# Kernel optimization log

Measured on AMD Instinct MI355X. Metric: run time of the kernel, lower is better.

Reference implementation:

```python
import jax, jax.numpy as jnp
import numpy as np

NUM_HEADS = 64  # from init_kwargs


def _rx(theta):
    # RX(theta) = [[cos(t/2), -i sin(t/2)], [-i sin(t/2), cos(t/2)]]
    theta = jnp.asarray(theta, jnp.float32)
    c = jnp.cos(theta / 2)
    s = jnp.sin(theta / 2)
    return jnp.stack([jnp.stack([c + 0j, -1j * s], -1),
                      jnp.stack([-1j * s, c + 0j], -1)], -2).astype(jnp.complex64)


def _ry(theta):
    # RY(theta) = [[cos(t/2), -sin(t/2)], [sin(t/2), cos(t/2)]]
    theta = jnp.asarray(theta, jnp.float32)
    c = jnp.cos(theta / 2)
    s = jnp.sin(theta / 2)
    return jnp.stack([jnp.stack([c + 0j, -s + 0j], -1),
                      jnp.stack([s + 0j, c + 0j], -1)], -2).astype(jnp.complex64)


def _apply_1q(state, U, wire):
    # state: (N, 2, 2, ..., 2) with wire w on axis 1+w (torchquantum convention)
    s = jnp.moveaxis(state, 1 + wire, -1)
    if U.ndim == 2:
        s = jnp.einsum('...i,ji->...j', s, U)
    else:  # per-sample gate, U: (N, 2, 2)
        s = jnp.einsum('n...i,nji->n...j', s, U)
    return jnp.moveaxis(s, -1, 1 + wire)


def _cnot(state, c, t):
    s = jnp.moveaxis(state, (1 + c, 1 + t), (-2, -1))
    s = s.at[..., 1, :].set(s[..., 1, ::-1])  # flip target where control==1
    return jnp.moveaxis(s, (-2, -1), (1 + c, 1 + t))


def _qlayer(xf, qparams):
    # xf: (N, d_k) angles; simulates RX-encode, per-wire RY/RX, CNOT ring, PauliZ expvals
    N, dk = xf.shape
    state = jnp.zeros((N, 2 ** dk), jnp.complex64).at[:, 0].set(1.0)
    state = state.reshape((N,) + (2,) * dk)
    for i in range(dk):                      # GeneralEncoder: RX(x_i) on wire i
        state = _apply_1q(state, _rx(xf[:, i]), i)
    for i in range(dk):                      # variational RY, RX per wire
        state = _apply_1q(state, _ry(qparams[i, 0]), i)
        state = _apply_1q(state, _rx(qparams[i, 1]), i)
    for i in range(dk - 1):                  # CNOT chain
        state = _cnot(state, i, i + 1)
    state = _cnot(state, dk - 1, 0)          # ring closure
    probs = state.real ** 2 + state.imag ** 2  # (N, 2,..,2)
    probs = probs.reshape(N, -1)
    # wire w is bit (dk-1-w) of the flattened index (wire 0 = MSB)
    bits = ((jnp.arange(2 ** dk)[:, None] >> jnp.arange(dk - 1, -1, -1)[None, :]) & 1).astype(jnp.float32)
    return probs @ (1.0 - 2.0 * bits)        # (N, dk) PauliZ expectations


def setup_inputs() -> dict:
    key = jax.random.key(0)
    ks = jax.random.split(key, 6)
    B, T, E, dk = 2, 512, 384, 384 // NUM_HEADS
    sc = 1.0 / np.sqrt(E)
    return {
        'x': jax.random.normal(ks[0], (B, T, E), jnp.float32),
        'Wq': jax.random.normal(ks[1], (E, E), jnp.float32) * sc,
        'bq': jnp.zeros((E,), jnp.float32),
        'Wk': jax.random.normal(ks[2], (E, E), jnp.float32) * sc,
        'bk': jnp.zeros((E,), jnp.float32),
        'Wv': jax.random.normal(ks[3], (E, E), jnp.float32) * sc,
        'bv': jnp.zeros((E,), jnp.float32),
        'Wo': jax.random.normal(ks[4], (E, E), jnp.float32) * sc,
        'bo': jnp.zeros((E,), jnp.float32),
        'qparams': jax.random.normal(ks[5], (dk, 2), jnp.float32),
    }


def reference(x, Wq, bq, Wk, bk, Wv, bv, Wo, bo, qparams):
    B, T, E = x.shape
    H = NUM_HEADS
    dk = E // H

    def heads(y):  # (B,T,E) -> (B,H,T,dk)
        return y.reshape(B, T, H, dk).transpose(0, 2, 1, 3)

    q = heads(x @ Wq.T + bq)
    k = heads(x @ Wk.T + bk)
    v = heads(x @ Wv.T + bv)

    def apply_q(layer):
        flat = layer.reshape(-1, dk)
        return _qlayer(flat, qparams).reshape(B, H, T, dk)

    qq, kq, vq = apply_q(q), apply_q(k), apply_q(v)
    scores = jnp.einsum('bhtd,bhsd->bhts', qq, kq) / jnp.sqrt(jnp.float32(dk))
    attn = jax.nn.softmax(scores, axis=-1)
    out = jnp.einsum('bhts,bhsd->bhtd', attn, vq)
    merged = out.transpose(0, 2, 1, 3).reshape(B, T, E)
    return merged @ Wo.T + bo
```

## Files before the change

### kernel.cpp

```cpp
#include <hip/hip_runtime.h>
#include <math.h>

#define SEQ_T   512
#define E_DIM   384
#define H_NUM   64
#define DKQ     6
#define NROWS   1024
#define QKV_ELEMS (NROWS*E_DIM)

__device__ __forceinline__ void qmap6(const float* __restrict__ in,
                                      const float* __restrict__ AB,
                                      float* __restrict__ out)
{
    float z[6];
#pragma unroll
    for (int i = 0; i < 6; ++i) {
        float s, c;
        sincosf(in[i], &s, &c);
        z[i] = AB[i] * c - AB[6 + i] * s;
    }
    float z01 = z[0] * z[1];
    float z12 = z[1] * z[2];
    float z34 = z[3] * z[4];
    out[0] = z12 * z34 * z[5];
    out[1] = z01;
    out[2] = z01 * z[2];
    out[3] = out[2] * z[3];
    out[4] = out[3] * z[4];
    out[5] = out[4] * z[5];
}

__global__ __launch_bounds__(256)
void qkv_gemm(const float* __restrict__ x,
              const float* __restrict__ Wq, const float* __restrict__ bq,
              const float* __restrict__ Wk, const float* __restrict__ bk,
              const float* __restrict__ Wv, const float* __restrict__ bv,
              float* __restrict__ qb, float* __restrict__ kb, float* __restrict__ vb)
{
    __shared__ float xs[64][65];
    __shared__ float ws[64][65];
    const int tid = threadIdx.x;
    const int tx = tid & 15;
    const int ty = tid >> 4;
    const int n0 = blockIdx.x * 64;
    const int j0 = blockIdx.y * 64;

    const float* W; const float* bias; float* ob; int e0;
    if (j0 < 384)      { W = Wq; bias = bq; ob = qb; e0 = j0; }
    else if (j0 < 768) { W = Wk; bias = bk; ob = kb; e0 = j0 - 384; }
    else               { W = Wv; bias = bv; ob = vb; e0 = j0 - 768; }

    float acc[4][4];
#pragma unroll
    for (int i = 0; i < 4; ++i)
#pragma unroll
        for (int j = 0; j < 4; ++j) acc[i][j] = 0.f;

    const int lrow = tid >> 4;
    const int lk   = (tid & 15) << 2;

    for (int kc = 0; kc < E_DIM; kc += 64) {
#pragma unroll
        for (int rr = 0; rr < 4; ++rr) {
            const int row = lrow + rr * 16;
            float4 xv = *reinterpret_cast<const float4*>(x + (size_t)(n0 + row) * E_DIM + kc + lk);
            xs[row][lk + 0] = xv.x; xs[row][lk + 1] = xv.y;
            xs[row][lk + 2] = xv.z; xs[row][lk + 3] = xv.w;
            float4 wv = *reinterpret_cast<const float4*>(W + (size_t)(e0 + row) * E_DIM + kc + lk);
            ws[row][lk + 0] = wv.x; ws[row][lk + 1] = wv.y;
            ws[row][lk + 2] = wv.z; ws[row][lk + 3] = wv.w;
        }
        __syncthreads();
#pragma unroll 8
        for (int kk = 0; kk < 64; ++kk) {
            float a0 = xs[ty * 4 + 0][kk], a1 = xs[ty * 4 + 1][kk];
            float a2 = xs[ty * 4 + 2][kk], a3 = xs[ty * 4 + 3][kk];
            float b0 = ws[tx * 4 + 0][kk], b1 = ws[tx * 4 + 1][kk];
            float b2 = ws[tx * 4 + 2][kk], b3 = ws[tx * 4 + 3][kk];
            acc[0][0] += a0 * b0; acc[0][1] += a0 * b1; acc[0][2] += a0 * b2; acc[0][3] += a0 * b3;
            acc[1][0] += a1 * b0; acc[1][1] += a1 * b1; acc[1][2] += a1 * b2; acc[1][3] += a1 * b3;
            acc[2][0] += a2 * b0; acc[2][1] += a2 * b1; acc[2][2] += a2 * b2; acc[2][3] += a2 * b3;
            acc[3][0] += a3 * b0; acc[3][1] += a3 * b1; acc[3][2] += a3 * b2; acc[3][3] += a3 * b3;
        }
        __syncthreads();
    }

#pragma unroll
    for (int i = 0; i < 4; ++i) {
        const int n = n0 + ty * 4 + i;
        const int b = n >> 9;
        const int t = n & 511;
#pragma unroll
        for (int j = 0; j < 4; ++j) {
            const int e = e0 + tx * 4 + j;
            const int h = e / 6;
            const int d = e - h * 6;
            const float v = acc[i][j] + bias[e];
            ob[(((size_t)(b * H_NUM + h) * SEQ_T) + t) * DKQ + d] = v;
        }
    }
}

__global__ __launch_bounds__(256)
void attn_kernel(const float* __restrict__ qb,
                 const float* __restrict__ kb,
                 const float* __restrict__ vb,
                 const float* __restrict__ qparams,
                 float* __restrict__ merged)
{
    __shared__ __align__(16) float kv[SEQ_T][12];

    const int bh  = blockIdx.x;
    const int tid = threadIdx.x;

    float AB[12];
#pragma unroll
    for (int i = 0; i < 6; ++i) {
        const float a = qparams[i * 2 + 0];
        const float b = qparams[i * 2 + 1];
        AB[i]     = cosf(a) * cosf(b);
        AB[6 + i] = sinf(b);
    }

    const float* Kp = kb + (size_t)bh * SEQ_T * DKQ;
    const float* Vp = vb + (size_t)bh * SEQ_T * DKQ;

    const int t = blockIdx.y * 256 + tid;
    float qin[6];
    const float* Qp = qb + ((size_t)bh * SEQ_T + t) * DKQ;
#pragma unroll
    for (int i = 0; i < 6; ++i) qin[i] = Qp[i];

    {
        const int p = tid;
        const float4* K4 = reinterpret_cast<const float4*>(Kp);
        const float4* V4 = reinterpret_cast<const float4*>(Vp);
        float4 ka = K4[3 * p + 0], kbv = K4[3 * p + 1], kc = K4[3 * p + 2];
        float4 va = V4[3 * p + 0], vbv = V4[3 * p + 1], vc = V4[3 * p + 2];

        float in0[6] = {ka.x, ka.y, ka.z, ka.w, kbv.x, kbv.y};
        float in1[6] = {kbv.z, kbv.w, kc.x, kc.y, kc.z, kc.w};
        float iv0[6] = {va.x, va.y, va.z, va.w, vbv.x, vbv.y};
        float iv1[6] = {vbv.z, vbv.w, vc.x, vc.y, vc.z, vc.w};
        float ok0[6], ok1[6], ov0[6], ov1[6];
        qmap6(in0, AB, ok0); qmap6(in1, AB, ok1);
        qmap6(iv0, AB, ov0); qmap6(iv1, AB, ov1);

        float4* kv4 = reinterpret_cast<float4*>(&kv[0][0]);
        kv4[3 * (2 * p) + 0] = make_float4(ok0[0], ok0[1], ok0[2], ok0[3]);
        kv4[3 * (2 * p) + 1] = make_float4(ok0[4], ok0[5], ov0[0], ov0[1]);
        kv4[3 * (2 * p) + 2] = make_float4(ov0[2], ov0[3], ov0[4], ov0[5]);
        kv4[3 * (2 * p + 1) + 0] = make_float4(ok1[0], ok1[1], ok1[2], ok1[3]);
        kv4[3 * (2 * p + 1) + 1] = make_float4(ok1[4], ok1[5], ov1[0], ov1[1]);
        kv4[3 * (2 * p + 1) + 2] = make_float4(ov1[2], ov1[3], ov1[4], ov1[5]);
    }
    __syncthreads();

    float qrow[6];
    qmap6(qin, AB, qrow);
    const float inv_sqrt_dk = 0.40824829046386296f;
#pragma unroll
    for (int i = 0; i < 6; ++i) qrow[i] *= inv_sqrt_dk;

    float accv[6] = {0.f, 0.f, 0.f, 0.f, 0.f, 0.f};
    float denom = 0.f;

    const float4* kv4 = reinterpret_cast<const float4*>(&kv[0][0]);
#pragma unroll 4
    for (int s = 0; s < SEQ_T; ++s) {
        const float4 r0 = kv4[3 * s + 0];
        const float4 r1 = kv4[3 * s + 1];
        const float4 r2 = kv4[3 * s + 2];
        const float sc = qrow[0] * r0.x + qrow[1] * r0.y + qrow[2] * r0.z
                       + qrow[3] * r0.w + qrow[4] * r1.x + qrow[5] * r1.y;
        const float e = __expf(sc);
        denom += e;
        accv[0] += e * r1.z; accv[1] += e * r1.w;
        accv[2] += e * r2.x; accv[3] += e * r2.y;
        accv[4] += e * r2.z; accv[5] += e * r2.w;
    }

    const float r = 1.0f / denom;
    const int b = bh >> 6;
    const int h = bh & 63;
    float* mp = merged + ((size_t)(b * SEQ_T + t)) * E_DIM + h * DKQ;
#pragma unroll
    for (int d = 0; d < 6; ++d) mp[d] = accv[d] * r;
}

__global__ __launch_bounds__(256)
void out_gemm(const float* __restrict__ merged,
              const float* __restrict__ Wo, const float* __restrict__ bo,
              float* __restrict__ out)
{
    __shared__ float xs[64][65];
    __shared__ float ws[64][65];
    const int tid = threadIdx.x;
    const int tx = tid & 15;
    const int ty = tid >> 4;
    const int n0 = blockIdx.x * 64;
    const int e0 = blockIdx.y * 64;

    float acc[4][4];
#pragma unroll
    for (int i = 0; i < 4; ++i)
#pragma unroll
        for (int j = 0; j < 4; ++j) acc[i][j] = 0.f;

    const int lrow = tid >> 4;
    const int lk   = (tid & 15) << 2;

    for (int kc = 0; kc < E_DIM; kc += 64) {
#pragma unroll
        for (int rr = 0; rr < 4; ++rr) {
            const int row = lrow + rr * 16;
            float4 xv = *reinterpret_cast<const float4*>(merged + (size_t)(n0 + row) * E_DIM + kc + lk);
            xs[row][lk + 0] = xv.x; xs[row][lk + 1] = xv.y;
            xs[row][lk + 2] = xv.z; xs[row][lk + 3] = xv.w;
            float4 wv = *reinterpret_cast<const float4*>(Wo + (size_t)(e0 + row) * E_DIM + kc + lk);
            ws[row][lk + 0] = wv.x; ws[row][lk + 1] = wv.y;
            ws[row][lk + 2] = wv.z; ws[row][lk + 3] = wv.w;
        }
        __syncthreads();
#pragma unroll 8
        for (int kk = 0; kk < 64; ++kk) {
            float a0 = xs[ty * 4 + 0][kk], a1 = xs[ty * 4 + 1][kk];
            float a2 = xs[ty * 4 + 2][kk], a3 = xs[ty * 4 + 3][kk];
            float b0 = ws[tx * 4 + 0][kk], b1 = ws[tx * 4 + 1][kk];
            float b2 = ws[tx * 4 + 2][kk], b3 = ws[tx * 4 + 3][kk];
            acc[0][0] += a0 * b0; acc[0][1] += a0 * b1; acc[0][2] += a0 * b2; acc[0][3] += a0 * b3;
            acc[1][0] += a1 * b0; acc[1][1] += a1 * b1; acc[1][2] += a1 * b2; acc[1][3] += a1 * b3;
            acc[2][0] += a2 * b0; acc[2][1] += a2 * b1; acc[2][2] += a2 * b2; acc[2][3] += a2 * b3;
            acc[3][0] += a3 * b0; acc[3][1] += a3 * b1; acc[3][2] += a3 * b2; acc[3][3] += a3 * b3;
        }
        __syncthreads();
    }

#pragma unroll
    for (int i = 0; i < 4; ++i) {
        const int n = n0 + ty * 4 + i;
#pragma unroll
        for (int j = 0; j < 4; ++j) {
            const int e = e0 + tx * 4 + j;
            out[(size_t)n * E_DIM + e] = acc[i][j] + bo[e];
        }
    }
}

extern "C" void kernel_launch(void* const* d_in, const int* in_sizes, int n_in,
                              void* d_out, int out_size, void* d_ws, size_t ws_size,
                              hipStream_t stream)
{
    const float* x  = (const float*)d_in[0];
    const float* Wq = (const float*)d_in[1];
    const float* bq = (const float*)d_in[2];
    const float* Wk = (const float*)d_in[3];
    const float* bk = (const float*)d_in[4];
    const float* Wv = (const float*)d_in[5];
    const float* bv = (const float*)d_in[6];
    const float* Wo = (const float*)d_in[7];
    const float* bo = (const float*)d_in[8];
    const float* qp = (const float*)d_in[9];
    float* out = (float*)d_out;

    float* qb     = (float*)d_ws;
    float* kb     = qb + QKV_ELEMS;
    float* vb     = kb + QKV_ELEMS;
    float* merged = vb + QKV_ELEMS;

    qkv_gemm<<<dim3(16, 18), 256, 0, stream>>>(x, Wq, bq, Wk, bk, Wv, bv, qb, kb, vb);
    attn_kernel<<<dim3(128, 2), 256, 0, stream>>>(qb, kb, vb, qp, merged);
    out_gemm<<<dim3(16, 6), 256, 0, stream>>>(merged, Wo, bo, out);
}
```

Measured before the change: 165.3 us.

## Split attention over key chunks, precompute quantum map, retile GEMMs to 32x48

Both GEMMs are retiled to 32x48 outputs per 64-thread block with transposed shared-memory layouts and vector loads, which raises the block count and aligns output columns to whole heads for vectorized stores. The quantum map is applied once in a separate in-place pass over qb, kb and vb, so attention no longer recomputes it per block. Attention becomes a split-K design: each block handles a 128-key chunk for all 512 queries and writes partial sums, and a reduce kernel combines the chunks without max subtraction. This adds two kernel launches and a round trip of partial sums through global memory in exchange for more parallelism.

```diff
diff --git a/kernel.cpp b/kernel.cpp
--- a/kernel.cpp
+++ b/kernel.cpp
@@ -7,6 +7,7 @@
 #define DKQ     6
 #define NROWS   1024
 #define QKV_ELEMS (NROWS*E_DIM)
+#define NCHUNK  4
 
 __device__ __forceinline__ void qmap6(const float* __restrict__ in,
                                       const float* __restrict__ AB,
@@ -30,89 +31,114 @@
     out[5] = out[4] * z[5];
 }
 
-__global__ __launch_bounds__(256)
+__device__ __forceinline__ void gemm_32x48(const float* __restrict__ A,
+                                           const float* __restrict__ W,
+                                           int n0, int e0,
+                                           float (&xs)[64][36], float (&ws)[64][52],
+                                           float (&acc)[4][6])
+{
+    const int tid = threadIdx.x;
+    const int tx = tid & 7;
+    const int ty = tid >> 3;
+
+#pragma unroll
+    for (int i = 0; i < 4; ++i)
+#pragma unroll
+        for (int j = 0; j < 6; ++j) acc[i][j] = 0.f;
+
+    for (int kc = 0; kc < E_DIM; kc += 64) {
+#pragma unroll
+        for (int w = 0; w < 8; ++w) {
+            const int idx = tid + 64 * w;
+            const int row = idx & 31;
+            const int kf  = idx >> 5;
+            const float4 g = *reinterpret_cast<const float4*>(
+                A + (size_t)(n0 + row) * E_DIM + kc + kf * 4);
+            xs[kf * 4 + 0][row] = g.x;
+            xs[kf * 4 + 1][row] = g.y;
+            xs[kf * 4 + 2][row] = g.z;
+            xs[kf * 4 + 3][row] = g.w;
+        }
+#pragma unroll
+        for (int w = 0; w < 12; ++w) {
+            const int idx = tid + 64 * w;
+            const int c  = idx % 48;
+            const int kf = idx / 48;
+            const float4 g = *reinterpret_cast<const float4*>(
+                W + (size_t)(e0 + c) * E_DIM + kc + kf * 4);
+            ws[kf * 4 + 0][c] = g.x;
+            ws[kf * 4 + 1][c] = g.y;
+            ws[kf * 4 + 2][c] = g.z;
+            ws[kf * 4 + 3][c] = g.w;
+        }
+        __syncthreads();
+
+#pragma unroll 8
+        for (int kk = 0; kk < 64; ++kk) {
+            const float4 a = *reinterpret_cast<const float4*>(&xs[kk][ty * 4]);
+            const float2 b0 = *reinterpret_cast<const float2*>(&ws[kk][tx * 6 + 0]);
+            const float2 b1 = *reinterpret_cast<const float2*>(&ws[kk][tx * 6 + 2]);
+            const float2 b2 = *reinterpret_cast<const float2*>(&ws[kk][tx * 6 + 4]);
+            const float av[4] = {a.x, a.y, a.z, a.w};
+            const float bv[6] = {b0.x, b0.y, b1.x, b1.y, b2.x, b2.y};
+#pragma unroll
+            for (int i = 0; i < 4; ++i)
+#pragma unroll
+                for (int j = 0; j < 6; ++j) acc[i][j] += av[i] * bv[j];
+        }
+        __syncthreads();
+    }
+}
+
+__global__ __launch_bounds__(64)
 void qkv_gemm(const float* __restrict__ x,
               const float* __restrict__ Wq, const float* __restrict__ bq,
               const float* __restrict__ Wk, const float* __restrict__ bk,
               const float* __restrict__ Wv, const float* __restrict__ bv,
               float* __restrict__ qb, float* __restrict__ kb, float* __restrict__ vb)
 {
-    __shared__ float xs[64][65];
-    __shared__ float ws[64][65];
-    const int tid = threadIdx.x;
-    const int tx = tid & 15;
-    const int ty = tid >> 4;
-    const int n0 = blockIdx.x * 64;
-    const int j0 = blockIdx.y * 64;
-
-    const float* W; const float* bias; float* ob; int e0;
-    if (j0 < 384)      { W = Wq; bias = bq; ob = qb; e0 = j0; }
-    else if (j0 < 768) { W = Wk; bias = bk; ob = kb; e0 = j0 - 384; }
-    else               { W = Wv; bias = bv; ob = vb; e0 = j0 - 768; }
-
-    float acc[4][4];
-#pragma unroll
-    for (int i = 0; i < 4; ++i)
-#pragma unroll
-        for (int j = 0; j < 4; ++j) acc[i][j] = 0.f;
-
-    const int lrow = tid >> 4;
-    const int lk   = (tid & 15) << 2;
-
-    for (int kc = 0; kc < E_DIM; kc += 64) {
-#pragma unroll
-        for (int rr = 0; rr < 4; ++rr) {
-            const int row = lrow + rr * 16;
-            float4 xv = *reinterpret_cast<const float4*>(x + (size_t)(n0 + row) * E_DIM + kc + lk);
-            xs[row][lk + 0] = xv.x; xs[row][lk + 1] = xv.y;
-            xs[row][lk + 2] = xv.z; xs[row][lk + 3] = xv.w;
-            float4 wv = *reinterpret_cast<const float4*>(W + (size_t)(e0 + row) * E_DIM + kc + lk);
-            ws[row][lk + 0] = wv.x; ws[row][lk + 1] = wv.y;
-            ws[row][lk + 2] = wv.z; ws[row][lk + 3] = wv.w;
-        }
-        __syncthreads();
-#pragma unroll 8
-        for (int kk = 0; kk < 64; ++kk) {
-            float a0 = xs[ty * 4 + 0][kk], a1 = xs[ty * 4 + 1][kk];
-            float a2 = xs[ty * 4 + 2][kk], a3 = xs[ty * 4 + 3][kk];
-            float b0 = ws[tx * 4 + 0][kk], b1 = ws[tx * 4 + 1][kk];
-            float b2 = ws[tx * 4 + 2][kk], b3 = ws[tx * 4 + 3][kk];
-            acc[0][0] += a0 * b0; acc[0][1] += a0 * b1; acc[0][2] += a0 * b2; acc[0][3] += a0 * b3;
-            acc[1][0] += a1 * b0; acc[1][1] += a1 * b1; acc[1][2] += a1 * b2; acc[1][3] += a1 * b3;
-            acc[2][0] += a2 * b0; acc[2][1] += a2 * b1; acc[2][2] += a2 * b2; acc[2][3] += a2 * b3;
-            acc[3][0] += a3 * b0; acc[3][1] += a3 * b1; acc[3][2] += a3 * b2; acc[3][3] += a3 * b3;
-        }
-        __syncthreads();
-    }
+    __shared__ __align__(16) float xs[64][36];
+    __shared__ __align__(16) float ws[64][52];
+
+    const int n0 = blockIdx.x * 32;
+    const int by = blockIdx.y;
+    const int sel = by >> 3;
+    const int e0 = (by & 7) * 48;
+
+    const float* W; const float* bias; float* ob;
+    if (sel == 0)      { W = Wq; bias = bq; ob = qb; }
+    else if (sel == 1) { W = Wk; bias = bk; ob = kb; }
+    else               { W = Wv; bias = bv; ob = vb; }
+
+    float acc[4][6];
+    gemm_32x48(x, W, n0, e0, xs, ws, acc);
+
+    const int tx = threadIdx.x & 7;
+    const int ty = threadIdx.x >> 3;
+    const int h = (e0 / 6) + tx;
+    const float2 bi0 = *reinterpret_cast<const float2*>(bias + e0 + tx * 6 + 0);
+    const float2 bi1 = *reinterpret_cast<const float2*>(bias + e0 + tx * 6 + 2);
+    const float2 bi2 = *reinterpret_cast<const float2*>(bias + e0 + tx * 6 + 4);
 
 #pragma unroll
     for (int i = 0; i < 4; ++i) {
         const int n = n0 + ty * 4 + i;
         const int b = n >> 9;
         const int t = n & 511;
-#pragma unroll
-        for (int j = 0; j < 4; ++j) {
-            const int e = e0 + tx * 4 + j;
-            const int h = e / 6;
-            const int d = e - h * 6;
-            const float v = acc[i][j] + bias[e];
-            ob[(((size_t)(b * H_NUM + h) * SEQ_T) + t) * DKQ + d] = v;
-        }
+        float* rp = ob + (((size_t)(b * H_NUM + h) * SEQ_T) + t) * DKQ;
+        float2 w0 = {acc[i][0] + bi0.x, acc[i][1] + bi0.y};
+        float2 w1 = {acc[i][2] + bi1.x, acc[i][3] + bi1.y};
+        float2 w2 = {acc[i][4] + bi2.x, acc[i][5] + bi2.y};
+        *reinterpret_cast<float2*>(rp + 0) = w0;
+        *reinterpret_cast<float2*>(rp + 2) = w1;
+        *reinterpret_cast<float2*>(rp + 4) = w2;
     }
 }
 
 __global__ __launch_bounds__(256)
-void attn_kernel(const float* __restrict__ qb,
-                 const float* __restrict__ kb,
-                 const float* __restrict__ vb,
-                 const float* __restrict__ qparams,
-                 float* __restrict__ merged)
-{
-    __shared__ __align__(16) float kv[SEQ_T][12];
-
-    const int bh  = blockIdx.x;
-    const int tid = threadIdx.x;
-
+void qmap_inplace(float* __restrict__ qb, const float* __restrict__ qparams)
+{
+    const int pid = blockIdx.x * 256 + threadIdx.x;
     float AB[12];
 #pragma unroll
     for (int i = 0; i < 6; ++i) {
@@ -121,129 +147,154 @@
         AB[i]     = cosf(a) * cosf(b);
         AB[6 + i] = sinf(b);
     }
-
-    const float* Kp = kb + (size_t)bh * SEQ_T * DKQ;
-    const float* Vp = vb + (size_t)bh * SEQ_T * DKQ;
-
-    const int t = blockIdx.y * 256 + tid;
-    float qin[6];
-    const float* Qp = qb + ((size_t)bh * SEQ_T + t) * DKQ;
-#pragma unroll
-    for (int i = 0; i < 6; ++i) qin[i] = Qp[i];
+    float4* p = reinterpret_cast<float4*>(qb + (size_t)pid * 12);
+    float4 g0 = p[0], g1 = p[1], g2 = p[2];
+    float in0[6] = {g0.x, g0.y, g0.z, g0.w, g1.x, g1.y};
+    float in1[6] = {g1.z, g1.w, g2.x, g2.y, g2.z, g2.w};
+    float o0[6], o1[6];
+    qmap6(in0, AB, o0);
+    qmap6(in1, AB, o1);
+    p[0] = make_float4(o0[0], o0[1], o0[2], o0[3]);
+    p[1] = make_float4(o0[4], o0[5], o1[0], o1[1]);
+    p[2] = make_float4(o1[2], o1[3], o1[4], o1[5]);
+}
+
+__global__ __launch_bounds__(128)
+void attn_partial(const float* __restrict__ qb,
+                  const float* __restrict__ kb,
+                  const float* __restrict__ vb,
+                  float* __restrict__ part)
+{
+    __shared__ __align__(16) float kv[128][12];
+
+    const int bh = blockIdx.x;
+    const int c  = blockIdx.y;
+    const int t  = threadIdx.x;
 
     {
-        const int p = tid;
-        const float4* K4 = reinterpret_cast<const float4*>(Kp);
-        const float4* V4 = reinterpret_cast<const float4*>(Vp);
-        float4 ka = K4[3 * p + 0], kbv = K4[3 * p + 1], kc = K4[3 * p + 2];
-        float4 va = V4[3 * p + 0], vbv = V4[3 * p + 1], vc = V4[3 * p + 2];
-
-        float in0[6] = {ka.x, ka.y, ka.z, ka.w, kbv.x, kbv.y};
-        float in1[6] = {kbv.z, kbv.w, kc.x, kc.y, kc.z, kc.w};
-        float iv0[6] = {va.x, va.y, va.z, va.w, vbv.x, vbv.y};
-        float iv1[6] = {vbv.z, vbv.w, vc.x, vc.y, vc.z, vc.w};
-        float ok0[6], ok1[6], ov0[6], ov1[6];
-        qmap6(in0, AB, ok0); qmap6(in1, AB, ok1);
-        qmap6(iv0, AB, ov0); qmap6(iv1, AB, ov1);
-
-        float4* kv4 = reinterpret_cast<float4*>(&kv[0][0]);
-        kv4[3 * (2 * p) + 0] = make_float4(ok0[0], ok0[1], ok0[2], ok0[3]);
-        kv4[3 * (2 * p) + 1] = make_float4(ok0[4], ok0[5], ov0[0], ov0[1]);
-        kv4[3 * (2 * p) + 2] = make_float4(ov0[2], ov0[3], ov0[4], ov0[5]);
-        kv4[3 * (2 * p + 1) + 0] = make_float4(ok1[0], ok1[1], ok1[2], ok1[3]);
-        kv4[3 * (2 * p + 1) + 1] = make_float4(ok1[4], ok1[5], ov1[0], ov1[1]);
-        kv4[3 * (2 * p + 1) + 2] = make_float4(ov1[2], ov1[3], ov1[4], ov1[5]);
+        const float* kr = kb + ((size_t)bh * SEQ_T + c * 128 + t) * DKQ;
+        const float* vr = vb + ((size_t)bh * SEQ_T + c * 128 + t) * DKQ;
+        const float2 k0 = *reinterpret_cast<const float2*>(kr + 0);
+        const float2 k1 = *reinterpret_cast<const float2*>(kr + 2);
+        const float2 k2 = *reinterpret_cast<const float2*>(kr + 4);
+        const float2 v0 = *reinterpret_cast<const float2*>(vr + 0);
+        const float2 v1 = *reinterpret_cast<const float2*>(vr + 2);
+        const float2 v2 = *reinterpret_cast<const float2*>(vr + 4);
+        float4* kvp = reinterpret_cast<float4*>(&kv[t][0]);
+        kvp[0] = make_float4(k0.x, k0.y, k1.x, k1.y);
+        kvp[1] = make_float4(k2.x, k2.y, v0.x, v0.y);
+        kvp[2] = make_float4(v1.x, v1.y, v2.x, v2.y);
+    }
+
+    const float inv_sqrt_dk = 0.40824829046386296f;
+    float qrow[4][6];
+#pragma unroll
+    for (int r = 0; r < 4; ++r) {
+        const float* qp = qb + ((size_t)bh * SEQ_T + r * 128 + t) * DKQ;
+        const float2 q0 = *reinterpret_cast<const float2*>(qp + 0);
+        const float2 q1 = *reinterpret_cast<const float2*>(qp + 2);
+        const float2 q2 = *reinterpret_cast<const float2*>(qp + 4);
+        qrow[r][0] = q0.x * inv_sqrt_dk; qrow[r][1] = q0.y * inv_sqrt_dk;
+        qrow[r][2] = q1.x * inv_sqrt_dk; qrow[r][3] = q1.y * inv_sqrt_dk;
+        qrow[r][4] = q2.x * inv_sqrt_dk; qrow[r][5] = q2.y * inv_sqrt_dk;
     }
     __syncthreads();
 
-    float qrow[6];
-    qmap6(qin, AB, qrow);
-    const float inv_sqrt_dk = 0.40824829046386296f;
-#pragma unroll
-    for (int i = 0; i < 6; ++i) qrow[i] *= inv_sqrt_dk;
-
-    float accv[6] = {0.f, 0.f, 0.f, 0.f, 0.f, 0.f};
-    float denom = 0.f;
+    float accv[4][6];
+    float den[4] = {0.f, 0.f, 0.f, 0.f};
+#pragma unroll
+    for (int r = 0; r < 4; ++r)
+#pragma unroll
+        for (int d = 0; d < 6; ++d) accv[r][d] = 0.f;
 
     const float4* kv4 = reinterpret_cast<const float4*>(&kv[0][0]);
-#pragma unroll 4
-    for (int s = 0; s < SEQ_T; ++s) {
+#pragma unroll 2
+    for (int s = 0; s < 128; ++s) {
         const float4 r0 = kv4[3 * s + 0];
         const float4 r1 = kv4[3 * s + 1];
         const float4 r2 = kv4[3 * s + 2];
-        const float sc = qrow[0] * r0.x + qrow[1] * r0.y + qrow[2] * r0.z
-                       + qrow[3] * r0.w + qrow[4] * r1.x + qrow[5] * r1.y;
-        const float e = __expf(sc);
-        denom += e;
-        accv[0] += e * r1.z; accv[1] += e * r1.w;
-        accv[2] += e * r2.x; accv[3] += e * r2.y;
-        accv[4] += e * r2.z; accv[5] += e * r2.w;
-    }
-
-    const float r = 1.0f / denom;
+#pragma unroll
+        for (int r = 0; r < 4; ++r) {
+            const float sc = qrow[r][0] * r0.x + qrow[r][1] * r0.y + qrow[r][2] * r0.z
+                           + qrow[r][3] * r0.w + qrow[r][4] * r1.x + qrow[r][5] * r1.y;
+            const float e = __expf(sc);
+            den[r] += e;
+            accv[r][0] += e * r1.z; accv[r][1] += e * r1.w;
+            accv[r][2] += e * r2.x; accv[r][3] += e * r2.y;
+            accv[r][4] += e * r2.z; accv[r][5] += e * r2.w;
+        }
+    }
+
+#pragma unroll
+    for (int r = 0; r < 4; ++r) {
+        const int q = r * 128 + t;
+        float4* pp = reinterpret_cast<float4*>(
+            part + ((size_t)((c * SEQ_T + q) * 128 + bh)) * 8);
+        pp[0] = make_float4(accv[r][0], accv[r][1], accv[r][2], accv[r][3]);
+        pp[1] = make_float4(accv[r][4], accv[r][5], den[r], 0.f);
+    }
+}
+
+__global__ __launch_bounds__(256)
+void attn_reduce(const float* __restrict__ part, float* __restrict__ merged)
+{
+    const int idx = blockIdx.x * 256 + threadIdx.x;
+    const int bh = idx & 127;
+    const int q  = idx >> 7;
+
+    float acc[6] = {0.f, 0.f, 0.f, 0.f, 0.f, 0.f};
+    float den = 0.f;
+#pragma unroll
+    for (int c = 0; c < NCHUNK; ++c) {
+        const float4* pp = reinterpret_cast<const float4*>(
+            part + ((size_t)((c * SEQ_T + q) * 128 + bh)) * 8);
+        const float4 a = pp[0];
+        const float4 b = pp[1];
+        acc[0] += a.x; acc[1] += a.y; acc[2] += a.z; acc[3] += a.w;
+        acc[4] += b.x; acc[5] += b.y; den += b.z;
+    }
+    const float r = 1.0f / den;
     const int b = bh >> 6;
     const int h = bh & 63;
-    float* mp = merged + ((size_t)(b * SEQ_T + t)) * E_DIM + h * DKQ;
-#pragma unroll
-    for (int d = 0; d < 6; ++d) mp[d] = accv[d] * r;
-}
-
-__global__ __launch_bounds__(256)
+    float* mp = merged + ((size_t)(b * SEQ_T + q)) * E_DIM + h * DKQ;
+    float2 w0 = {acc[0] * r, acc[1] * r};
+    float2 w1 = {acc[2] * r, acc[3] * r};
+    float2 w2 = {acc[4] * r, acc[5] * r};
+    *reinterpret_cast<float2*>(mp + 0) = w0;
+    *reinterpret_cast<float2*>(mp + 2) = w1;
+    *reinterpret_cast<float2*>(mp + 4) = w2;
+}
+
+__global__ __launch_bounds__(64)
 void out_gemm(const float* __restrict__ merged,
               const float* __restrict__ Wo, const float* __restrict__ bo,
               float* __restrict__ out)
 {
-    __shared__ float xs[64][65];
-    __shared__ float ws[64][65];
-    const int tid = threadIdx.x;
-    const int tx = tid & 15;
-    const int ty = tid >> 4;
-    const int n0 = blockIdx.x * 64;
-    const int e0 = blockIdx.y * 64;
-
-    float acc[4][4];
-#pragma unroll
-    for (int i = 0; i < 4; ++i)
-#pragma unroll
-        for (int j = 0; j < 4; ++j) acc[i][j] = 0.f;
-
-    const int lrow = tid >> 4;
-    const int lk   = (tid & 15) << 2;
-
-    for (int kc = 0; kc < E_DIM; kc += 64) {
-#pragma unroll
-        for (int rr = 0; rr < 4; ++rr) {
-            const int row = lrow + rr * 16;
-            float4 xv = *reinterpret_cast<const float4*>(merged + (size_t)(n0 + row) * E_DIM + kc + lk);
-            xs[row][lk + 0] = xv.x; xs[row][lk + 1] = xv.y;
-            xs[row][lk + 2] = xv.z; xs[row][lk + 3] = xv.w;
-            float4 wv = *reinterpret_cast<const float4*>(Wo + (size_t)(e0 + row) * E_DIM + kc + lk);
-            ws[row][lk + 0] = wv.x; ws[row][lk + 1] = wv.y;
-            ws[row][lk + 2] = wv.z; ws[row][lk + 3] = wv.w;
-        }
-        __syncthreads();
-#pragma unroll 8
-        for (int kk = 0; kk < 64; ++kk) {
-            float a0 = xs[ty * 4 + 0][kk], a1 = xs[ty * 4 + 1][kk];
-            float a2 = xs[ty * 4 + 2][kk], a3 = xs[ty * 4 + 3][kk];
-            float b0 = ws[tx * 4 + 0][kk], b1 = ws[tx * 4 + 1][kk];
-            float b2 = ws[tx * 4 + 2][kk], b3 = ws[tx * 4 + 3][kk];
-            acc[0][0] += a0 * b0; acc[0][1] += a0 * b1; acc[0][2] += a0 * b2; acc[0][3] += a0 * b3;
-            acc[1][0] += a1 * b0; acc[1][1] += a1 * b1; acc[1][2] += a1 * b2; acc[1][3] += a1 * b3;
-            acc[2][0] += a2 * b0; acc[2][1] += a2 * b1; acc[2][2] += a2 * b2; acc[2][3] += a2 * b3;
-            acc[3][0] += a3 * b0; acc[3][1] += a3 * b1; acc[3][2] += a3 * b2; acc[3][3] += a3 * b3;
-        }
-        __syncthreads();
-    }
+    __shared__ __align__(16) float xs[64][36];
+    __shared__ __align__(16) float ws[64][52];
+
+    const int n0 = blockIdx.x * 32;
+    const int e0 = blockIdx.y * 48;
+
+    float acc[4][6];
+    gemm_32x48(merged, Wo, n0, e0, xs, ws, acc);
+
+    const int tx = threadIdx.x & 7;
+    const int ty = threadIdx.x >> 3;
+    const float2 bi0 = *reinterpret_cast<const float2*>(bo + e0 + tx * 6 + 0);
+    const float2 bi1 = *reinterpret_cast<const float2*>(bo + e0 + tx * 6 + 2);
+    const float2 bi2 = *reinterpret_cast<const float2*>(bo + e0 + tx * 6 + 4);
 
 #pragma unroll
     for (int i = 0; i < 4; ++i) {
         const int n = n0 + ty * 4 + i;
-#pragma unroll
-        for (int j = 0; j < 4; ++j) {
-            const int e = e0 + tx * 4 + j;
-            out[(size_t)n * E_DIM + e] = acc[i][j] + bo[e];
-        }
+        float* rp = out + (size_t)n * E_DIM + e0 + tx * 6;
+        float2 w0 = {acc[i][0] + bi0.x, acc[i][1] + bi0.y};
+        float2 w1 = {acc[i][2] + bi1.x, acc[i][3] + bi1.y};
+        float2 w2 = {acc[i][4] + bi2.x, acc[i][5] + bi2.y};
+        *reinterpret_cast<float2*>(rp + 0) = w0;
+        *reinterpret_cast<float2*>(rp + 2) = w1;
+        *reinterpret_cast<float2*>(rp + 4) = w2;
     }
 }
 
@@ -267,8 +318,11 @@
     float* kb     = qb + QKV_ELEMS;
     float* vb     = kb + QKV_ELEMS;
     float* merged = vb + QKV_ELEMS;
-
-    qkv_gemm<<<dim3(16, 18), 256, 0, stream>>>(x, Wq, bq, Wk, bk, Wv, bv, qb, kb, vb);
-    attn_kernel<<<dim3(128, 2), 256, 0, stream>>>(qb, kb, vb, qp, merged);
-    out_gemm<<<dim3(16, 6), 256, 0, stream>>>(merged, Wo, bo, out);
-}
+    float* part   = merged + QKV_ELEMS;
+
+    qkv_gemm<<<dim3(32, 24), 64, 0, stream>>>(x, Wq, bq, Wk, bk, Wv, bv, qb, kb, vb);
+    qmap_inplace<<<384, 256, 0, stream>>>(qb, qp);
+    attn_partial<<<dim3(128, NCHUNK), 128, 0, stream>>>(qb, kb, vb, part);
+    attn_reduce<<<256, 256, 0, stream>>>(part, merged);
+    out_gemm<<<dim3(32, 8), 64, 0, stream>>>(merged, Wo, bo, out);
+}
```

New measurement: 166.7 us. Within noise of the previous version (+0.8%).
